# Kernel optimization log

Hardware: AMD Instinct MI355X
Metric: run time of the kernel (lower is better)

The kernel has to match this reference:

```python
import jax, jax.numpy as jnp
import numpy as np

N = 50000      # input_dim == output_dim
E = 800000     # nnz in sparse weight (original: 12300 from w_ind.mat)
B = 64         # batch


def setup_inputs() -> dict:
    key = jax.random.key(0)
    k1, k2, k3, k4, k5 = jax.random.split(key, 5)
    inputs = jax.random.normal(k1, (B, N), dtype=jnp.float32)
    # truncated-normal(std=0.01) approximated by scaled normal
    W3 = 0.01 * jax.random.normal(k2, (E,), dtype=jnp.float32)
    b = jnp.zeros((N,), dtype=jnp.float32)
    # velocity = 1250 * row of CSV -> positive scale vector
    velocity = 1250.0 * jax.random.uniform(k3, (N,), dtype=jnp.float32)
    I = jax.random.randint(k4, (E,), 0, N, dtype=jnp.int64)  # row (dest) index
    J = jax.random.randint(k5, (E,), 0, N, dtype=jnp.int64)  # col (source) index
    return {"inputs": inputs, "W3": W3, "b": b, "velocity": velocity, "I": I, "J": J}


def reference(inputs, W3, b, velocity, I, J):
    # sparse W[i,j] = W3[e] scaled by velocity broadcast along rows -> * velocity[J]
    wv = W3 * velocity[J]                       # [E]
    # out = (W_sparse @ inputs^T)^T + b  == scatter-add over rows I
    contrib = inputs[:, J] * wv[None, :]        # [B, E] gather + scale
    out = jnp.zeros((inputs.shape[0], velocity.shape[0]), inputs.dtype)
    out = out.at[:, I].add(contrib)             # [B, N] scatter-add
    return out + b
```

## Files before the change

kernel.cpp:

```cpp
#include <hip/hip_runtime.h>


#define BATCH 64
#define QROWS 64
#define PCHUNK 2048
#define GCH 512
#define BCAP 32
#define BSTR 33

typedef unsigned long long ull;

__global__ void k_prep(const float* __restrict__ in, float* __restrict__ in_T,
                       int* __restrict__ coarse_hist, int NC, int N) {
    const int gid = blockIdx.x * 256 + threadIdx.x;
    if (gid < NC) coarse_hist[gid] = 0;

    __shared__ float tile[64 * 65];
    const int n0 = blockIdx.x * 64;
    const int t  = threadIdx.x;
    const int x  = t & 63;
    const int r  = t >> 6;
    for (int b = r; b < BATCH; b += 4) {
        float v = 0.f;
        if (n0 + x < N) v = in[(size_t)b * N + n0 + x];
        tile[x * 65 + b] = v;
    }
    __syncthreads();
    for (int xr = r; xr < 64; xr += 4) {
        if (n0 + xr < N) in_T[(size_t)(n0 + xr) * BATCH + x] = tile[xr * 65 + x];
    }
}

__global__ void __launch_bounds__(512) k_hist(const int* __restrict__ I,
                                              int* __restrict__ coarse_hist,
                                              int E, int NC) {
    __shared__ int h[1024];
    const int t = threadIdx.x;
    for (int c = t; c < NC; c += 512) h[c] = 0;
    __syncthreads();
    const int e0 = blockIdx.x * PCHUNK;
    int e1 = e0 + PCHUNK; if (e1 > E) e1 = E;
    for (int e = e0 + t; e < e1; e += 512) atomicAdd(&h[I[e] >> 6], 1);
    __syncthreads();
    for (int c = t; c < NC; c += 512) if (h[c]) atomicAdd(&coarse_hist[c], h[c]);
}

__global__ void __launch_bounds__(1024) k_scan(const int* __restrict__ coarse_hist,
                                               int* __restrict__ coarse_base,
                                               int* __restrict__ gcursor, int NC) {
    __shared__ int sh[1024];
    const int t = threadIdx.x;
    const int v = (t < NC) ? coarse_hist[t] : 0;
    sh[t] = v;
    __syncthreads();
    for (int off = 1; off < 1024; off <<= 1) {
        const int u = (t >= off) ? sh[t - off] : 0;
        __syncthreads();
        sh[t] += u;
        __syncthreads();
    }
    if (t < NC) { coarse_base[t] = sh[t] - v; gcursor[t] = sh[t] - v; }
    if (t == NC - 1) coarse_base[NC] = sh[t];
}

__global__ void __launch_bounds__(512) k_partition(
        const int* __restrict__ I, const int* __restrict__ J,
        const float* __restrict__ W3, const float* __restrict__ velocity,
        int* __restrict__ gcursor, ull* __restrict__ part, int E, int NC) {
    __shared__ int hist[1024];
    __shared__ int base[1024];
    const int t = threadIdx.x;
    for (int c = t; c < NC; c += 512) hist[c] = 0;
    __syncthreads();
    const int e0 = blockIdx.x * PCHUNK;
    int e1 = e0 + PCHUNK; if (e1 > E) e1 = E;

    ull  rec[4];
    int  cb[4];
    int  rk[4];
    bool ok[4];
    #pragma unroll
    for (int u = 0; u < 4; ++u) {
        const int e = e0 + u * 512 + t;
        ok[u] = (e < e1);
        cb[u] = 0; rk[u] = 0; rec[u] = 0ull;
        if (ok[u]) {
            const int   i = I[e];
            const int   j = J[e];
            const float w = W3[e] * velocity[j];
            cb[u] = i >> 6;
            rk[u] = atomicAdd(&hist[cb[u]], 1);
            rec[u] = ((ull)__float_as_uint(w) << 32)
                   | ((ull)((unsigned)(i & 63) << 16) | (unsigned)j);
        }
    }
    __syncthreads();
    for (int c = t; c < NC; c += 512) {
        const int cnt = hist[c];
        base[c] = cnt ? atomicAdd(&gcursor[c], cnt) : 0;
    }
    __syncthreads();
    #pragma unroll
    for (int u = 0; u < 4; ++u)
        if (ok[u]) part[(size_t)base[cb[u]] + rk[u]] = rec[u];
}

__global__ void __launch_bounds__(512) k_gather(
        const float* __restrict__ in_T, const ull* __restrict__ part,
        const int* __restrict__ coarse_base, const float* __restrict__ bias,
        float* __restrict__ out, int N) {
    __shared__ ull smem[64 * BSTR + GCH];
    __shared__ int cnt[64];
    __shared__ int ocnt;
    ull* const bins = smem;
    ull* const ovf  = smem + 64 * BSTR;
    float* const tile = (float*)smem;

    const int t    = threadIdx.x;
    const int lane = t & 63;
    const int w    = t >> 6;
    const int c    = blockIdx.x;

    const int beg = coarse_base[c];
    const int end = coarse_base[c + 1];

    float acc[8];
    #pragma unroll
    for (int r = 0; r < 8; ++r) acc[r] = 0.f;

    for (int cb = beg; cb < end; cb += GCH) {
        __syncthreads();
        if (t < 64) cnt[t] = 0;
        if (t == 0) ocnt = 0;
        __syncthreads();

        const int e = cb + t;
        if (e < end) {
            const ull rec = part[e];
            const int li = (int)(((unsigned)rec >> 16) & 63u);
            const int r = atomicAdd(&cnt[li], 1);
            if (r < BCAP) bins[li * BSTR + r] = rec;
            else          ovf[atomicAdd(&ocnt, 1)] = rec;
        }
        __syncthreads();

        #pragma unroll
        for (int r8 = 0; r8 < 8; ++r8) {
            const int row = w * 8 + r8;
            int n = cnt[row]; if (n > BCAP) n = BCAP;
            const ull* bp = &bins[row * BSTR];
            float a = acc[r8];
            int k = 0;
            for (; k + 4 <= n; k += 4) {
                const ull r0 = bp[k], r1 = bp[k + 1], r2 = bp[k + 2], r3 = bp[k + 3];
                const float v0 = in_T[(int)((unsigned)r0 & 0xffffu) * BATCH + lane];
                const float v1 = in_T[(int)((unsigned)r1 & 0xffffu) * BATCH + lane];
                const float v2 = in_T[(int)((unsigned)r2 & 0xffffu) * BATCH + lane];
                const float v3 = in_T[(int)((unsigned)r3 & 0xffffu) * BATCH + lane];
                a += v0 * __uint_as_float((unsigned)(r0 >> 32));
                a += v1 * __uint_as_float((unsigned)(r1 >> 32));
                a += v2 * __uint_as_float((unsigned)(r2 >> 32));
                a += v3 * __uint_as_float((unsigned)(r3 >> 32));
            }
            for (; k < n; ++k) {
                const ull rr = bp[k];
                a += in_T[(int)((unsigned)rr & 0xffffu) * BATCH + lane]
                   * __uint_as_float((unsigned)(rr >> 32));
            }
            acc[r8] = a;
        }

        const int oc = ocnt;
        if (oc > 0) {
            #pragma unroll
            for (int r8 = 0; r8 < 8; ++r8) {
                const int row = w * 8 + r8;
                float a = acc[r8];
                for (int k = 0; k < oc; ++k) {
                    const ull rr = ovf[k];
                    if ((int)(((unsigned)rr >> 16) & 63u) == row)
                        a += in_T[(int)((unsigned)rr & 0xffffu) * BATCH + lane]
                           * __uint_as_float((unsigned)(rr >> 32));
                }
                acc[r8] = a;
            }
        }
    }

    __syncthreads();
    #pragma unroll
    for (int r8 = 0; r8 < 8; ++r8)
        tile[(w * 8 + r8) * 65 + lane] = acc[r8];
    __syncthreads();

    const int n0  = c * QROWS;
    const int row = t & 63;
    const int bq  = t >> 6;
    const int n = n0 + row;
    if (n < N) {
        const float bv = bias[n];
        for (int b = bq; b < BATCH; b += 8)
            out[(size_t)b * N + n] = tile[row * 65 + b] + bv;
    }
}

__global__ void k_edge_scatter_direct(const float* __restrict__ in,
                                      const float* __restrict__ W3,
                                      const float* __restrict__ velocity,
                                      const int* __restrict__ I,
                                      const int* __restrict__ J,
                                      float* __restrict__ out, int N, int E) {
    const int lane = threadIdx.x & 63;
    const long wave   = (long)blockIdx.x * (blockDim.x >> 6) + (threadIdx.x >> 6);
    const long nwaves = (long)gridDim.x * (blockDim.x >> 6);
    for (long base = wave * 64; base < E; base += nwaves * 64) {
        const long e = base + lane;
        int iv = 0, jv = 0; float wvv = 0.f;
        if (e < E) { iv = I[e]; jv = J[e]; wvv = W3[e] * velocity[jv]; }
        const int cnt = (int)((E - base) < 64 ? (E - base) : 64);
        for (int k = 0; k < cnt; ++k) {
            const int   ii = __shfl(iv, k);
            const int   jj = __shfl(jv, k);
            const float wvx = __shfl(wvv, k);
            const float val = in[(size_t)lane * N + jj] * wvx;
            atomicAdd(&out[(size_t)lane * N + ii], val);
        }
    }
}

__global__ void k_add_bias(const float* __restrict__ bias, float* __restrict__ out, int N, int total) {
    int idx = blockIdx.x * blockDim.x + threadIdx.x;
    if (idx < total) out[idx] += bias[idx % N];
}

extern "C" void kernel_launch(void* const* d_in, const int* in_sizes, int n_in,
                              void* d_out, int out_size, void* d_ws, size_t ws_size,
                              hipStream_t stream) {
    const float* inputs   = (const float*)d_in[0];
    const float* W3       = (const float*)d_in[1];
    const float* bias     = (const float*)d_in[2];
    const float* velocity = (const float*)d_in[3];
    const int*   I        = (const int*)d_in[4];
    const int*   J        = (const int*)d_in[5];
    const int E = in_sizes[1];
    const int N = in_sizes[3];
    float* out = (float*)d_out;

    const size_t mat_elems = (size_t)N * BATCH;
    const int NC   = (N + QROWS - 1) / QROWS;
    const int nb_n = (N + 63) / 64;
    const int nb_e = (E + PCHUNK - 1) / PCHUNK;

    const size_t need = mat_elems * sizeof(float)
                      + (size_t)E * sizeof(ull)
                      + (size_t)(NC + (NC + 1) + NC) * sizeof(int);

    if (ws_size >= need && N <= 65535 && NC <= 1024) {
        float* in_T        = (float*)d_ws;
        ull*   part        = (ull*)(in_T + mat_elems);
        int*   coarse_hist = (int*)(part + E);
        int*   coarse_base = coarse_hist + NC;
        int*   gcursor     = coarse_base + NC + 1;

        k_prep     <<<nb_n, 256,  0, stream>>>(inputs, in_T, coarse_hist, NC, N);
        k_hist     <<<nb_e, 512,  0, stream>>>(I, coarse_hist, E, NC);
        k_scan     <<<1,    1024, 0, stream>>>(coarse_hist, coarse_base, gcursor, NC);
        k_partition<<<nb_e, 512,  0, stream>>>(I, J, W3, velocity, gcursor, part, E, NC);
        k_gather   <<<NC,   512,  0, stream>>>(in_T, part, coarse_base, bias, out, N);
    } else {
        hipMemsetAsync(out, 0, (size_t)out_size * sizeof(float), stream);
        const int waves_needed   = (E + 63) / 64;
        const int scatter_blocks = (waves_needed + 3) / 4;
        k_edge_scatter_direct<<<scatter_blocks, 256, 0, stream>>>(inputs, W3, velocity, I, J, out, N, E);
        k_add_bias<<<(out_size + 255) / 256, 256, 0, stream>>>(bias, out, N, out_size);
    }
}
```

Measured before the change: 148.9 us.

## Coarsen partition buckets to 256 rows, split gather per quarter, fuse prep with histogram

Edges are now partitioned into 256-row buckets instead of 64-row ones, which cuts the number of buckets and the global cursor atomics. The global cursors are padded to separate cache lines to reduce atomic contention. The gather launches four blocks per bucket, each filtering for its own 64-row quarter, so every block reads four times as much of the partition data as before. The transpose and histogram kernels are merged into one launch, with a memset zeroing the histogram. Bin capacity drops to 16, so more records may spill into the slower overflow path.

```diff
diff --git a/kernel.cpp b/kernel.cpp
--- a/kernel.cpp
+++ b/kernel.cpp
@@ -2,55 +2,53 @@
 
 
 #define BATCH 64
-#define QROWS 64
+#define RB 256
 #define PCHUNK 2048
 #define GCH 512
-#define BCAP 32
-#define BSTR 33
+#define BCAP 16
+#define BSTR 17
+#define GSTR 16
 
 typedef unsigned long long ull;
 
-__global__ void k_prep(const float* __restrict__ in, float* __restrict__ in_T,
-                       int* __restrict__ coarse_hist, int NC, int N) {
-    const int gid = blockIdx.x * 256 + threadIdx.x;
-    if (gid < NC) coarse_hist[gid] = 0;
-
+__global__ void __launch_bounds__(256) k_prep_hist(
+        const float* __restrict__ in, float* __restrict__ in_T,
+        const int* __restrict__ I, int* __restrict__ coarse_hist,
+        int NCB, int N, int E, int nb_n) {
     __shared__ float tile[64 * 65];
-    const int n0 = blockIdx.x * 64;
-    const int t  = threadIdx.x;
-    const int x  = t & 63;
-    const int r  = t >> 6;
-    for (int b = r; b < BATCH; b += 4) {
-        float v = 0.f;
-        if (n0 + x < N) v = in[(size_t)b * N + n0 + x];
-        tile[x * 65 + b] = v;
-    }
-    __syncthreads();
-    for (int xr = r; xr < 64; xr += 4) {
-        if (n0 + xr < N) in_T[(size_t)(n0 + xr) * BATCH + x] = tile[xr * 65 + x];
-    }
-}
-
-__global__ void __launch_bounds__(512) k_hist(const int* __restrict__ I,
-                                              int* __restrict__ coarse_hist,
-                                              int E, int NC) {
-    __shared__ int h[1024];
     const int t = threadIdx.x;
-    for (int c = t; c < NC; c += 512) h[c] = 0;
-    __syncthreads();
-    const int e0 = blockIdx.x * PCHUNK;
-    int e1 = e0 + PCHUNK; if (e1 > E) e1 = E;
-    for (int e = e0 + t; e < e1; e += 512) atomicAdd(&h[I[e] >> 6], 1);
-    __syncthreads();
-    for (int c = t; c < NC; c += 512) if (h[c]) atomicAdd(&coarse_hist[c], h[c]);
+
+    if ((int)blockIdx.x < nb_n) {
+        const int n0 = blockIdx.x * 64;
+        const int x  = t & 63;
+        const int r  = t >> 6;
+        for (int b = r; b < BATCH; b += 4) {
+            float v = 0.f;
+            if (n0 + x < N) v = in[(size_t)b * N + n0 + x];
+            tile[x * 65 + b] = v;
+        }
+        __syncthreads();
+        for (int xr = r; xr < 64; xr += 4) {
+            if (n0 + xr < N) in_T[(size_t)(n0 + xr) * BATCH + x] = tile[xr * 65 + x];
+        }
+    } else {
+        int* h = (int*)tile;
+        for (int c = t; c < NCB; c += 256) h[c] = 0;
+        __syncthreads();
+        const int e0 = ((int)blockIdx.x - nb_n) * PCHUNK;
+        int e1 = e0 + PCHUNK; if (e1 > E) e1 = E;
+        for (int e = e0 + t; e < e1; e += 256) atomicAdd(&h[I[e] >> 8], 1);
+        __syncthreads();
+        for (int c = t; c < NCB; c += 256) if (h[c]) atomicAdd(&coarse_hist[c], h[c]);
+    }
 }
 
 __global__ void __launch_bounds__(1024) k_scan(const int* __restrict__ coarse_hist,
                                                int* __restrict__ coarse_base,
-                                               int* __restrict__ gcursor, int NC) {
+                                               int* __restrict__ gcursor, int NCB) {
     __shared__ int sh[1024];
     const int t = threadIdx.x;
-    const int v = (t < NC) ? coarse_hist[t] : 0;
+    const int v = (t < NCB) ? coarse_hist[t] : 0;
     sh[t] = v;
     __syncthreads();
     for (int off = 1; off < 1024; off <<= 1) {
@@ -59,18 +57,18 @@
         sh[t] += u;
         __syncthreads();
     }
-    if (t < NC) { coarse_base[t] = sh[t] - v; gcursor[t] = sh[t] - v; }
-    if (t == NC - 1) coarse_base[NC] = sh[t];
+    if (t < NCB) { coarse_base[t] = sh[t] - v; gcursor[t * GSTR] = sh[t] - v; }
+    if (t == NCB - 1) coarse_base[NCB] = sh[t];
 }
 
 __global__ void __launch_bounds__(512) k_partition(
         const int* __restrict__ I, const int* __restrict__ J,
         const float* __restrict__ W3, const float* __restrict__ velocity,
-        int* __restrict__ gcursor, ull* __restrict__ part, int E, int NC) {
+        int* __restrict__ gcursor, ull* __restrict__ part, int E, int NCB) {
     __shared__ int hist[1024];
     __shared__ int base[1024];
     const int t = threadIdx.x;
-    for (int c = t; c < NC; c += 512) hist[c] = 0;
+    for (int c = t; c < NCB; c += 512) hist[c] = 0;
     __syncthreads();
     const int e0 = blockIdx.x * PCHUNK;
     int e1 = e0 + PCHUNK; if (e1 > E) e1 = E;
@@ -88,16 +86,16 @@
             const int   i = I[e];
             const int   j = J[e];
             const float w = W3[e] * velocity[j];
-            cb[u] = i >> 6;
+            cb[u] = i >> 8;
             rk[u] = atomicAdd(&hist[cb[u]], 1);
             rec[u] = ((ull)__float_as_uint(w) << 32)
-                   | ((ull)((unsigned)(i & 63) << 16) | (unsigned)j);
-        }
-    }
-    __syncthreads();
-    for (int c = t; c < NC; c += 512) {
+                   | ((ull)((unsigned)(i & 255) << 16) | (unsigned)j);
+        }
+    }
+    __syncthreads();
+    for (int c = t; c < NCB; c += 512) {
         const int cnt = hist[c];
-        base[c] = cnt ? atomicAdd(&gcursor[c], cnt) : 0;
+        base[c] = cnt ? atomicAdd(&gcursor[c * GSTR], cnt) : 0;
     }
     __syncthreads();
     #pragma unroll
@@ -109,7 +107,7 @@
         const float* __restrict__ in_T, const ull* __restrict__ part,
         const int* __restrict__ coarse_base, const float* __restrict__ bias,
         float* __restrict__ out, int N) {
-    __shared__ ull smem[64 * BSTR + GCH];
+    __shared__ ull smem[64 * 65 / 2];
     __shared__ int cnt[64];
     __shared__ int ocnt;
     ull* const bins = smem;
@@ -119,7 +117,8 @@
     const int t    = threadIdx.x;
     const int lane = t & 63;
     const int w    = t >> 6;
-    const int c    = blockIdx.x;
+    const int c    = blockIdx.x >> 2;
+    const unsigned q = blockIdx.x & 3;
 
     const int beg = coarse_base[c];
     const int end = coarse_base[c + 1];
@@ -137,10 +136,13 @@
         const int e = cb + t;
         if (e < end) {
             const ull rec = part[e];
-            const int li = (int)(((unsigned)rec >> 16) & 63u);
-            const int r = atomicAdd(&cnt[li], 1);
-            if (r < BCAP) bins[li * BSTR + r] = rec;
-            else          ovf[atomicAdd(&ocnt, 1)] = rec;
+            const unsigned lo = (unsigned)rec;
+            if (((lo >> 22) & 3u) == q) {
+                const int li = (int)((lo >> 16) & 63u);
+                const int r = atomicAdd(&cnt[li], 1);
+                if (r < BCAP) bins[li * BSTR + r] = rec;
+                else          ovf[atomicAdd(&ocnt, 1)] = rec;
+            }
         }
         __syncthreads();
 
@@ -193,7 +195,7 @@
         tile[(w * 8 + r8) * 65 + lane] = acc[r8];
     __syncthreads();
 
-    const int n0  = c * QROWS;
+    const int n0  = c * RB + (int)q * 64;
     const int row = t & 63;
     const int bq  = t >> 6;
     const int n = n0 + row;
@@ -247,26 +249,26 @@
     float* out = (float*)d_out;
 
     const size_t mat_elems = (size_t)N * BATCH;
-    const int NC   = (N + QROWS - 1) / QROWS;
+    const int NCB  = (N + RB - 1) / RB;
     const int nb_n = (N + 63) / 64;
     const int nb_e = (E + PCHUNK - 1) / PCHUNK;
 
     const size_t need = mat_elems * sizeof(float)
                       + (size_t)E * sizeof(ull)
-                      + (size_t)(NC + (NC + 1) + NC) * sizeof(int);
-
-    if (ws_size >= need && N <= 65535 && NC <= 1024) {
+                      + (size_t)(NCB + (NCB + 1) + NCB * GSTR) * sizeof(int);
+
+    if (ws_size >= need && N <= 65535 && NCB <= 1024) {
         float* in_T        = (float*)d_ws;
         ull*   part        = (ull*)(in_T + mat_elems);
         int*   coarse_hist = (int*)(part + E);
-        int*   coarse_base = coarse_hist + NC;
-        int*   gcursor     = coarse_base + NC + 1;
-
-        k_prep     <<<nb_n, 256,  0, stream>>>(inputs, in_T, coarse_hist, NC, N);
-        k_hist     <<<nb_e, 512,  0, stream>>>(I, coarse_hist, E, NC);
-        k_scan     <<<1,    1024, 0, stream>>>(coarse_hist, coarse_base, gcursor, NC);
-        k_partition<<<nb_e, 512,  0, stream>>>(I, J, W3, velocity, gcursor, part, E, NC);
-        k_gather   <<<NC,   512,  0, stream>>>(in_T, part, coarse_base, bias, out, N);
+        int*   coarse_base = coarse_hist + NCB;
+        int*   gcursor     = coarse_base + NCB + 1;
+
+        hipMemsetAsync(coarse_hist, 0, (size_t)NCB * sizeof(int), stream);
+        k_prep_hist<<<nb_n + nb_e, 256,  0, stream>>>(inputs, in_T, I, coarse_hist, NCB, N, E, nb_n);
+        k_scan     <<<1,           1024, 0, stream>>>(coarse_hist, coarse_base, gcursor, NCB);
+        k_partition<<<nb_e,        512,  0, stream>>>(I, J, W3, velocity, gcursor, part, E, NCB);
+        k_gather   <<<NCB * 4,     512,  0, stream>>>(in_T, part, coarse_base, bias, out, N);
     } else {
         hipMemsetAsync(out, 0, (size_t)out_size * sizeof(float), stream);
         const int waves_needed   = (E + 63) / 64;
```

Result: slower. 171.0 us (+14.8%).

## Fuse transpose and histogram kernels, fold velocity into transposed input, pad cursors

Applied to the files above, without the earlier changes.

Merges the input transpose and the coarse row histogram into one launch, with separate block ranges doing each job, and zeroes the histogram with a memset. Velocity scaling moves from a per-edge random gather in the partition kernel to a per-column multiply during the transpose, since velocity[J] scales column J of the input. The global cursors are padded to one per 64 bytes to reduce contention on shared cache lines during the partition atomics. This removes one kernel launch and E random velocity loads, at the cost of an extra memset and a larger cursor array.

```diff
diff --git a/kernel.cpp b/kernel.cpp
--- a/kernel.cpp
+++ b/kernel.cpp
@@ -7,42 +7,44 @@
 #define GCH 512
 #define BCAP 32
 #define BSTR 33
+#define GSTR 16
 
 typedef unsigned long long ull;
 
-__global__ void k_prep(const float* __restrict__ in, float* __restrict__ in_T,
-                       int* __restrict__ coarse_hist, int NC, int N) {
-    const int gid = blockIdx.x * 256 + threadIdx.x;
-    if (gid < NC) coarse_hist[gid] = 0;
-
+__global__ void __launch_bounds__(256) k_prep_hist(
+        const float* __restrict__ in, const float* __restrict__ velocity,
+        float* __restrict__ in_T,
+        const int* __restrict__ I, int* __restrict__ coarse_hist,
+        int NC, int N, int E, int nb_n) {
     __shared__ float tile[64 * 65];
-    const int n0 = blockIdx.x * 64;
-    const int t  = threadIdx.x;
-    const int x  = t & 63;
-    const int r  = t >> 6;
-    for (int b = r; b < BATCH; b += 4) {
-        float v = 0.f;
-        if (n0 + x < N) v = in[(size_t)b * N + n0 + x];
-        tile[x * 65 + b] = v;
-    }
-    __syncthreads();
-    for (int xr = r; xr < 64; xr += 4) {
-        if (n0 + xr < N) in_T[(size_t)(n0 + xr) * BATCH + x] = tile[xr * 65 + x];
-    }
-}
-
-__global__ void __launch_bounds__(512) k_hist(const int* __restrict__ I,
-                                              int* __restrict__ coarse_hist,
-                                              int E, int NC) {
-    __shared__ int h[1024];
     const int t = threadIdx.x;
-    for (int c = t; c < NC; c += 512) h[c] = 0;
-    __syncthreads();
-    const int e0 = blockIdx.x * PCHUNK;
-    int e1 = e0 + PCHUNK; if (e1 > E) e1 = E;
-    for (int e = e0 + t; e < e1; e += 512) atomicAdd(&h[I[e] >> 6], 1);
-    __syncthreads();
-    for (int c = t; c < NC; c += 512) if (h[c]) atomicAdd(&coarse_hist[c], h[c]);
+
+    if ((int)blockIdx.x < nb_n) {
+        const int n0 = blockIdx.x * 64;
+        const int x  = t & 63;
+        const int r  = t >> 6;
+        for (int b = r; b < BATCH; b += 4) {
+            float v = 0.f;
+            if (n0 + x < N) v = in[(size_t)b * N + n0 + x];
+            tile[x * 65 + b] = v;
+        }
+        __syncthreads();
+        for (int xr = r; xr < 64; xr += 4) {
+            if (n0 + xr < N) {
+                const float vel = velocity[n0 + xr];
+                in_T[(size_t)(n0 + xr) * BATCH + x] = tile[xr * 65 + x] * vel;
+            }
+        }
+    } else {
+        int* h = (int*)tile;
+        for (int c = t; c < NC; c += 256) h[c] = 0;
+        __syncthreads();
+        const int e0 = ((int)blockIdx.x - nb_n) * PCHUNK;
+        int e1 = e0 + PCHUNK; if (e1 > E) e1 = E;
+        for (int e = e0 + t; e < e1; e += 256) atomicAdd(&h[I[e] >> 6], 1);
+        __syncthreads();
+        for (int c = t; c < NC; c += 256) if (h[c]) atomicAdd(&coarse_hist[c], h[c]);
+    }
 }
 
 __global__ void __launch_bounds__(1024) k_scan(const int* __restrict__ coarse_hist,
@@ -59,13 +61,13 @@
         sh[t] += u;
         __syncthreads();
     }
-    if (t < NC) { coarse_base[t] = sh[t] - v; gcursor[t] = sh[t] - v; }
+    if (t < NC) { coarse_base[t] = sh[t] - v; gcursor[t * GSTR] = sh[t] - v; }
     if (t == NC - 1) coarse_base[NC] = sh[t];
 }
 
 __global__ void __launch_bounds__(512) k_partition(
         const int* __restrict__ I, const int* __restrict__ J,
-        const float* __restrict__ W3, const float* __restrict__ velocity,
+        const float* __restrict__ W3,
         int* __restrict__ gcursor, ull* __restrict__ part, int E, int NC) {
     __shared__ int hist[1024];
     __shared__ int base[1024];
@@ -85,19 +87,18 @@
         ok[u] = (e < e1);
         cb[u] = 0; rk[u] = 0; rec[u] = 0ull;
         if (ok[u]) {
-            const int   i = I[e];
-            const int   j = J[e];
-            const float w = W3[e] * velocity[j];
+            const int i = I[e];
+            const int j = J[e];
             cb[u] = i >> 6;
             rk[u] = atomicAdd(&hist[cb[u]], 1);
-            rec[u] = ((ull)__float_as_uint(w) << 32)
+            rec[u] = ((ull)__float_as_uint(W3[e]) << 32)
                    | ((ull)((unsigned)(i & 63) << 16) | (unsigned)j);
         }
     }
     __syncthreads();
     for (int c = t; c < NC; c += 512) {
         const int cnt = hist[c];
-        base[c] = cnt ? atomicAdd(&gcursor[c], cnt) : 0;
+        base[c] = cnt ? atomicAdd(&gcursor[c * GSTR], cnt) : 0;
     }
     __syncthreads();
     #pragma unroll
@@ -253,7 +254,7 @@
 
     const size_t need = mat_elems * sizeof(float)
                       + (size_t)E * sizeof(ull)
-                      + (size_t)(NC + (NC + 1) + NC) * sizeof(int);
+                      + (size_t)(NC + (NC + 1) + NC * GSTR) * sizeof(int);
 
     if (ws_size >= need && N <= 65535 && NC <= 1024) {
         float* in_T        = (float*)d_ws;
@@ -262,11 +263,11 @@
         int*   coarse_base = coarse_hist + NC;
         int*   gcursor     = coarse_base + NC + 1;
 
-        k_prep     <<<nb_n, 256,  0, stream>>>(inputs, in_T, coarse_hist, NC, N);
-        k_hist     <<<nb_e, 512,  0, stream>>>(I, coarse_hist, E, NC);
-        k_scan     <<<1,    1024, 0, stream>>>(coarse_hist, coarse_base, gcursor, NC);
-        k_partition<<<nb_e, 512,  0, stream>>>(I, J, W3, velocity, gcursor, part, E, NC);
-        k_gather   <<<NC,   512,  0, stream>>>(in_T, part, coarse_base, bias, out, N);
+        hipMemsetAsync(coarse_hist, 0, (size_t)NC * sizeof(int), stream);
+        k_prep_hist<<<nb_n + nb_e, 256,  0, stream>>>(inputs, velocity, in_T, I, coarse_hist, NC, N, E, nb_n);
+        k_scan     <<<1,           1024, 0, stream>>>(coarse_hist, coarse_base, gcursor, NC);
+        k_partition<<<nb_e,        512,  0, stream>>>(I, J, W3, gcursor, part, E, NC);
+        k_gather   <<<NC,          512,  0, stream>>>(in_T, part, coarse_base, bias, out, N);
     } else {
         hipMemsetAsync(out, 0, (size_t)out_size * sizeof(float), stream);
         const int waves_needed   = (E + 63) / 64;
```

Result: slower. 156.5 us (+5.1%).
